# Kernel tuning notes

Measured on AMD Instinct MI355X. Metric: run time of the kernel, lower is better.

The kernel has to match this reference:

```python
import jax, jax.numpy as jnp
import numpy as np

DT = 1.0
SPIKE_THRESHOLD = 30.0


def setup_inputs() -> dict:
    key = jax.random.key(0)
    kx, = jax.random.split(key, 1)
    x = jax.random.normal(kx, (16, 64, 1024, 32), dtype=jnp.float32)
    # scalar learnable parameters (Izhikevich model constants)
    a = jnp.float32(0.02)
    b = jnp.float32(0.2)
    c = jnp.float32(-65.0)
    d = jnp.float32(8.0)
    return {"x": x, "a": a, "b": b, "c": c, "d": d}


def reference(x, a, b, c, d):
    # x: [B, C, N, T]. Initial membrane potential v and recovery u are zeros.
    B, C, N, T = x.shape
    v0 = jnp.zeros((B, C, N), dtype=x.dtype)
    u0 = jnp.zeros((B, C, N), dtype=x.dtype)
    xs = jnp.moveaxis(x, -1, 0)  # [T, B, C, N] time-major for scan

    def step(carry, x_t):
        v, u = carry
        dv = 0.04 * v * v + 5.0 * v + 140.0 - u + x_t
        v = v + DT * dv
        du = a * (b * v - u)
        u = u + DT * du
        spike = (v >= SPIKE_THRESHOLD).astype(x_t.dtype)
        v = v * (1.0 - spike) + c * spike
        u = u + d * spike
        return (v, u), spike

    (_, _), spikes = jax.lax.scan(step, (v0, u0), xs)
    return jnp.moveaxis(spikes, 0, -1)  # [B, C, N, T]
```

## Files before the change

### kernel.cpp

```cpp
#include <hip/hip_runtime.h>


#define T_STEPS 32

__global__ __launch_bounds__(256) void izhikevich_kernel(
    const float* __restrict__ x,
    const float* __restrict__ pa,
    const float* __restrict__ pb,
    const float* __restrict__ pc,
    const float* __restrict__ pd,
    float* __restrict__ out,
    int n_neurons)
{
#pragma clang fp contract(off)
    const int n = blockIdx.x * blockDim.x + threadIdx.x;
    if (n >= n_neurons) return;

    const float a = pa[0];
    const float b = pb[0];
    const float c = pc[0];
    const float d = pd[0];

    const float4* __restrict__ xp =
        reinterpret_cast<const float4*>(x + (size_t)n * T_STEPS);
    float4* __restrict__ op =
        reinterpret_cast<float4*>(out + (size_t)n * T_STEPS);

    float4 xs[8];
#pragma unroll
    for (int k = 0; k < 8; ++k) xs[k] = xp[k];
    const float* xf = reinterpret_cast<const float*>(xs);

    float v = 0.0f;
    float u = 0.0f;

#pragma unroll
    for (int k = 0; k < 8; ++k) {
        float4 sp;
        float* sf = reinterpret_cast<float*>(&sp);
#pragma unroll
        for (int j = 0; j < 4; ++j) {
            const float xt = xf[k * 4 + j];
            const float t1 = (0.04f * v) * v;
            const float t2 = 5.0f * v;
            const float dv = (((t1 + t2) + 140.0f) - u) + xt;
            v = v + dv;
            const float du = a * ((b * v) - u);
            u = u + du;
            const float spike = (v >= 30.0f) ? 1.0f : 0.0f;
            const float oms = 1.0f - spike;
            v = (v * oms) + (c * spike);
            u = u + (d * spike);
            sf[j] = spike;
        }
        op[k] = sp;
    }
}

extern "C" void kernel_launch(void* const* d_in, const int* in_sizes, int n_in,
                              void* d_out, int out_size, void* d_ws, size_t ws_size,
                              hipStream_t stream) {
    const float* x  = (const float*)d_in[0];
    const float* pa = (const float*)d_in[1];
    const float* pb = (const float*)d_in[2];
    const float* pc = (const float*)d_in[3];
    const float* pd = (const float*)d_in[4];
    float* out = (float*)d_out;

    const int n_neurons = in_sizes[0] / T_STEPS;
    const int block = 256;
    const int grid = (n_neurons + block - 1) / block;

    izhikevich_kernel<<<grid, block, 0, stream>>>(x, pa, pb, pc, pd, out,
                                                  n_neurons);
}
```

Before: 265.1 us.

## Coalesce loads via LDS transpose with software-pipelined multi-tile wavefronts

Each 64-thread block now handles four tiles of 64 neurons. It loads every tile with fully coalesced dwordx4 inline-asm loads, transposes the data through XOR-swizzled shared memory so each lane holds one neuron's 32 timesteps, and transposes the spikes back before doing coalesced stores. Loads for the next tile are double-buffered and overlapped with compute using manual vmcnt waits. This targets the strided per-thread 128-byte accesses of the original. In exchange it adds LDS traffic, hand-written asm that bypasses compiler scheduling, and assumes the neuron count divides evenly into tiles, with no bounds checks.

```diff
diff --git a/kernel.cpp b/kernel.cpp
--- a/kernel.cpp
+++ b/kernel.cpp
@@ -1,60 +1,142 @@
 #include <hip/hip_runtime.h>
 
 
-#define T_STEPS 32
+typedef float v4f __attribute__((ext_vector_type(4)));
 
-__global__ __launch_bounds__(256) void izhikevich_kernel(
+#define TPB 64
+#define ITERS 4
+
+__global__ __launch_bounds__(TPB) void izhikevich_kernel(
     const float* __restrict__ x,
     const float* __restrict__ pa,
     const float* __restrict__ pb,
     const float* __restrict__ pc,
     const float* __restrict__ pd,
     float* __restrict__ out,
-    int n_neurons)
+    int stride_tiles)
 {
 #pragma clang fp contract(off)
-    const int n = blockIdx.x * blockDim.x + threadIdx.x;
-    if (n >= n_neurons) return;
+    __shared__ float L[2048];
+
+    const int lane = threadIdx.x;
+    const int oct  = lane >> 3;
+    const int grp  = lane & 7;
+    const int scat_base = oct * 32 + ((grp ^ oct) << 2);
+    const int row_base  = lane * 32;
 
     const float a = pa[0];
     const float b = pb[0];
     const float c = pc[0];
     const float d = pd[0];
+    asm volatile("" :: "v"(a), "v"(b), "v"(c), "v"(d));
 
-    const float4* __restrict__ xp =
-        reinterpret_cast<const float4*>(x + (size_t)n * T_STEPS);
-    float4* __restrict__ op =
-        reinterpret_cast<float4*>(out + (size_t)n * T_STEPS);
+    const int off0 = lane * 16;
+    const int off4 = off0 + 4096;
 
-    float4 xs[8];
-#pragma unroll
-    for (int k = 0; k < 8; ++k) xs[k] = xp[k];
-    const float* xf = reinterpret_cast<const float*>(xs);
+    const int wid = blockIdx.x;
 
-    float v = 0.0f;
-    float u = 0.0f;
+    v4f A0, A1, A2, A3, A4, A5, A6, A7;
+    v4f B0, B1, B2, B3, B4, B5, B6, B7;
 
-#pragma unroll
-    for (int k = 0; k < 8; ++k) {
-        float4 sp;
-        float* sf = reinterpret_cast<float*>(&sp);
-#pragma unroll
-        for (int j = 0; j < 4; ++j) {
-            const float xt = xf[k * 4 + j];
-            const float t1 = (0.04f * v) * v;
-            const float t2 = 5.0f * v;
-            const float dv = (((t1 + t2) + 140.0f) - u) + xt;
-            v = v + dv;
-            const float du = a * ((b * v) - u);
-            u = u + du;
-            const float spike = (v >= 30.0f) ? 1.0f : 0.0f;
-            const float oms = 1.0f - spike;
-            v = (v * oms) + (c * spike);
-            u = u + (d * spike);
-            sf[j] = spike;
-        }
-        op[k] = sp;
-    }
+#define LOAD8(basep, r0, r1, r2, r3, r4, r5, r6, r7)                        \
+    asm volatile(                                                           \
+        "global_load_dwordx4 %0, %8, %10 offset:0\n\t"                      \
+        "global_load_dwordx4 %1, %8, %10 offset:1024\n\t"                   \
+        "global_load_dwordx4 %2, %8, %10 offset:2048\n\t"                   \
+        "global_load_dwordx4 %3, %8, %10 offset:3072\n\t"                   \
+        "global_load_dwordx4 %4, %9, %10 offset:0\n\t"                      \
+        "global_load_dwordx4 %5, %9, %10 offset:1024\n\t"                   \
+        "global_load_dwordx4 %6, %9, %10 offset:2048\n\t"                   \
+        "global_load_dwordx4 %7, %9, %10 offset:3072"                       \
+        : "=&v"(r0), "=&v"(r1), "=&v"(r2), "=&v"(r3),                       \
+          "=&v"(r4), "=&v"(r5), "=&v"(r6), "=&v"(r7)                        \
+        : "v"(off0), "v"(off4), "s"(basep))
+
+#define WAITVM(n) asm volatile("s_waitcnt vmcnt(" #n ")" ::: "memory")
+
+#define PROCESS(tile, r0, r1, r2, r3, r4, r5, r6, r7)                       \
+    do {                                                                    \
+        *reinterpret_cast<v4f*>(&L[0 * 256 + scat_base]) = r0;              \
+        *reinterpret_cast<v4f*>(&L[1 * 256 + scat_base]) = r1;              \
+        *reinterpret_cast<v4f*>(&L[2 * 256 + scat_base]) = r2;              \
+        *reinterpret_cast<v4f*>(&L[3 * 256 + scat_base]) = r3;              \
+        *reinterpret_cast<v4f*>(&L[4 * 256 + scat_base]) = r4;              \
+        *reinterpret_cast<v4f*>(&L[5 * 256 + scat_base]) = r5;              \
+        *reinterpret_cast<v4f*>(&L[6 * 256 + scat_base]) = r6;              \
+        *reinterpret_cast<v4f*>(&L[7 * 256 + scat_base]) = r7;              \
+        v4f xs[8];                                                          \
+        _Pragma("unroll")                                                   \
+        for (int q = 0; q < 8; ++q)                                         \
+            xs[q] = *reinterpret_cast<const v4f*>(                          \
+                &L[row_base + ((q ^ grp) << 2)]);                           \
+        float* xf = reinterpret_cast<float*>(xs);                           \
+        float v = 0.0f;                                                     \
+        float u = 0.0f;                                                     \
+        _Pragma("unroll")                                                   \
+        for (int j = 0; j < 32; ++j) {                                      \
+            const float xt = xf[j];                                         \
+            const float t1 = (0.04f * v) * v;                               \
+            const float t2 = 5.0f * v;                                      \
+            const float dv = (((t1 + t2) + 140.0f) - u) + xt;               \
+            v = v + dv;                                 \
+            const float du = a * ((b * v) - u);                             \
+            u = u + du;                                                     \
+            const float spike = (v >= 30.0f) ? 1.0f : 0.0f;                 \
+            const float oms = 1.0f - spike;                                 \
+            v = (v * oms) + (c * spike);         \
+            u = u + (d * spike);                                            \
+            xf[j] = spike;                       \
+        }                                                                   \
+        _Pragma("unroll")                                                   \
+        for (int q = 0; q < 8; ++q)                                         \
+            *reinterpret_cast<v4f*>(&L[row_base + ((q ^ grp) << 2)]) =      \
+                xs[q];                                                      \
+        v4f o0 = *reinterpret_cast<const v4f*>(&L[0 * 256 + scat_base]);    \
+        v4f o1 = *reinterpret_cast<const v4f*>(&L[1 * 256 + scat_base]);    \
+        v4f o2 = *reinterpret_cast<const v4f*>(&L[2 * 256 + scat_base]);    \
+        v4f o3 = *reinterpret_cast<const v4f*>(&L[3 * 256 + scat_base]);    \
+        v4f o4 = *reinterpret_cast<const v4f*>(&L[4 * 256 + scat_base]);    \
+        v4f o5 = *reinterpret_cast<const v4f*>(&L[5 * 256 + scat_base]);    \
+        v4f o6 = *reinterpret_cast<const v4f*>(&L[6 * 256 + scat_base]);    \
+        v4f o7 = *reinterpret_cast<const v4f*>(&L[7 * 256 + scat_base]);    \
+        const float* obase = out + (size_t)(tile) * 2048;                   \
+        asm volatile(                                                       \
+            "global_store_dwordx4 %8, %0, %10 offset:0\n\t"                 \
+            "global_store_dwordx4 %8, %1, %10 offset:1024\n\t"              \
+            "global_store_dwordx4 %8, %2, %10 offset:2048\n\t"              \
+            "global_store_dwordx4 %8, %3, %10 offset:3072\n\t"              \
+            "global_store_dwordx4 %9, %4, %10 offset:0\n\t"                 \
+            "global_store_dwordx4 %9, %5, %10 offset:1024\n\t"              \
+            "global_store_dwordx4 %9, %6, %10 offset:2048\n\t"              \
+            "global_store_dwordx4 %9, %7, %10 offset:3072"                  \
+            :                                                               \
+            : "v"(o0), "v"(o1), "v"(o2), "v"(o3),                           \
+              "v"(o4), "v"(o5), "v"(o6), "v"(o7),                           \
+              "v"(off0), "v"(off4), "s"(obase)                              \
+            : "memory");                                                    \
+    } while (0)
+
+    const int s1 = stride_tiles;
+    LOAD8(x + (size_t)wid * 2048, A0, A1, A2, A3, A4, A5, A6, A7);
+
+    LOAD8(x + (size_t)(wid + s1) * 2048, B0, B1, B2, B3, B4, B5, B6, B7);
+    WAITVM(8);
+    PROCESS(wid, A0, A1, A2, A3, A4, A5, A6, A7);
+
+    LOAD8(x + (size_t)(wid + 2 * s1) * 2048, A0, A1, A2, A3, A4, A5, A6, A7);
+    WAITVM(8);
+    PROCESS(wid + s1, B0, B1, B2, B3, B4, B5, B6, B7);
+
+    LOAD8(x + (size_t)(wid + 3 * s1) * 2048, B0, B1, B2, B3, B4, B5, B6, B7);
+    WAITVM(8);
+    PROCESS(wid + 2 * s1, A0, A1, A2, A3, A4, A5, A6, A7);
+
+    WAITVM(0);
+    PROCESS(wid + 3 * s1, B0, B1, B2, B3, B4, B5, B6, B7);
+
+#undef LOAD8
+#undef WAITVM
+#undef PROCESS
 }
 
 extern "C" void kernel_launch(void* const* d_in, const int* in_sizes, int n_in,
@@ -67,10 +149,11 @@
     const float* pd = (const float*)d_in[4];
     float* out = (float*)d_out;
 
-    const int n_neurons = in_sizes[0] / T_STEPS;
-    const int block = 256;
-    const int grid = (n_neurons + block - 1) / block;
+    const int n_neurons = in_sizes[0] / 32;
+    const int n_tiles = n_neurons / 64;
+    const int grid = n_tiles / ITERS;
+    const int stride_tiles = grid;
 
-    izhikevich_kernel<<<grid, block, 0, stream>>>(x, pa, pb, pc, pd, out,
-                                                  n_neurons);
+    izhikevich_kernel<<<grid, TPB, 0, stream>>>(x, pa, pb, pc, pd, out,
+                                                stride_tiles);
 }
```

Measured after the change: 242.5 us. -8.5%, faster.
